# Optimization experiments

Hardware: AMD Instinct MI355X
Metric: run time of the kernel (lower is better)

Reference implementation:

```python
import jax, jax.numpy as jnp
import numpy as np

IN_F, OUT_F, R = 4096, 4096, 16
SCALING = 32.0 / R  # lora_alpha / r


def setup_inputs() -> dict:
    key = jax.random.key(0)
    kx, kw, kb, ka, kB = jax.random.split(key, 5)
    bound_w = 1.0 / np.sqrt(IN_F)  # kaiming_uniform a=sqrt(5) on (out,in) -> U(-1/sqrt(in), 1/sqrt(in))
    x = jax.random.normal(kx, (4, 4096, IN_F), dtype=jnp.float32)
    weight = jax.random.uniform(kw, (OUT_F, IN_F), jnp.float32, -bound_w, bound_w)
    bias = jax.random.uniform(kb, (OUT_F,), jnp.float32, -bound_w, bound_w)
    lora_A = jax.random.uniform(ka, (R, IN_F), jnp.float32, -bound_w, bound_w)
    # B is zero-init in the module; use small random values so the LoRA path is exercised
    lora_B = jax.random.normal(kB, (OUT_F, R), dtype=jnp.float32) * 0.01
    return {"x": x, "weight": weight, "bias": bias, "lora_A": lora_A, "lora_B": lora_B}


def reference(x, weight, bias, lora_A, lora_B):
    # base: F.linear(x, W, b) = x @ W.T + b
    base_out = jnp.einsum("bsi,oi->bso", x, weight) + bias
    # low-rank path: (x @ A.T) @ B.T * scaling  (dropout=0 -> identity)
    xr = jnp.einsum("bsi,ri->bsr", x, lora_A)  # [b, s, r]
    lora_out = jnp.einsum("bsr,or->bso", xr, lora_B) * SCALING
    return base_out + lora_out
```

## Files before the change

### kernel.cpp

```cpp
#include <hip/hip_runtime.h>
#include <hip/hip_bf16.h>


typedef __attribute__((ext_vector_type(8))) short bf16x8;
typedef __attribute__((ext_vector_type(4))) float f32x4;
typedef __attribute__((ext_vector_type(4))) unsigned short u16x4;

#define M_DIM 16384
#define N_DIM 4096
#define K_DIM 4096
#define NT 64

__device__ __forceinline__ unsigned short f2bf(float f) {
    unsigned int u = __builtin_bit_cast(unsigned int, f);
    unsigned int r = u + 0x7FFFu + ((u >> 16) & 1u);
    return (unsigned short)(r >> 16);
}

__device__ __forceinline__ void async16(const void* g, void* l) {
    __builtin_amdgcn_global_load_lds(
        (const __attribute__((address_space(1))) unsigned int*)g,
        (__attribute__((address_space(3))) unsigned int*)l,
        16, 0, 0);
}

__global__ void __launch_bounds__(256) cast_x_kernel(
    const float4* __restrict__ x, u16x4* __restrict__ y, int n4) {
    int i = blockIdx.x * blockDim.x + threadIdx.x;
    int stride = gridDim.x * blockDim.x;
    for (; i < n4; i += stride) {
        float4 v = x[i];
        u16x4 o = { f2bf(v.x), f2bf(v.y), f2bf(v.z), f2bf(v.w) };
        y[i] = o;
    }
}

__global__ void __launch_bounds__(256) weff_kernel(
    const float* __restrict__ W, const float* __restrict__ lA,
    const float* __restrict__ lB, unsigned short* __restrict__ out) {
    constexpr int K = K_DIM, R = 16;
    constexpr float S = 2.0f;
    int o = blockIdx.x;
    int t = threadIdx.x;
    float b[R];
#pragma unroll
    for (int r = 0; r < R; ++r) b[r] = lB[o * R + r];
#pragma unroll
    for (int c = 0; c < 4; ++c) {
        int i = c * 1024 + t * 4;
        float4 wv = *reinterpret_cast<const float4*>(&W[o * K + i]);
        float sx = 0.f, sy = 0.f, sz = 0.f, sw = 0.f;
#pragma unroll
        for (int r = 0; r < R; ++r) {
            float4 a = *reinterpret_cast<const float4*>(&lA[r * K + i]);
            sx += b[r] * a.x; sy += b[r] * a.y;
            sz += b[r] * a.z; sw += b[r] * a.w;
        }
        u16x4 ov = { f2bf(wv.x + S * sx), f2bf(wv.y + S * sy),
                     f2bf(wv.z + S * sz), f2bf(wv.w + S * sw) };
        *reinterpret_cast<u16x4*>(&out[o * K + i]) = ov;
    }
}

#define STAGE(G, h, tt, bsel, moff)                                           \
    do {                                                                      \
        const unsigned short* g0 = (G) +                                      \
            (size_t)((h) * 128 + wid * 16 + rc) * K_DIM + (tt) * 64 + cc * 8; \
        char* l0 = lds + (bsel) * 65536 + (moff) + (h) * 16384 + wid * 2048;  \
        async16(g0, l0);                                                      \
        async16(g0 + 8 * K_DIM, l0 + 1024);                                   \
    } while (0)

#define LDA_TO(dst, mh, bsel)                                                 \
    _Pragma("unroll") for (int mm = 0; mm < 4; ++mm)                          \
    _Pragma("unroll") for (int ks = 0; ks < 2; ++ks)                          \
        dst[mm][ks] = *(const bf16x8*)(lds + (bsel) * 65536 +                 \
            ((aBase + ((mh) * 4 + mm) * 2048) ^ (ks << 6)));

#define LDB_TO(nh, bsel)                                                      \
    _Pragma("unroll") for (int nn = 0; nn < 2; ++nn)                          \
    _Pragma("unroll") for (int ks = 0; ks < 2; ++ks)                          \
        br[(nh) * 2 + nn][ks] = *(const bf16x8*)(lds + (bsel) * 65536 +       \
            ((bBase + ((nh) * 2 + nn) * 2048) ^ (ks << 6)));

#define MM_Q(src, mh, nh)                                                     \
    __builtin_amdgcn_s_setprio(1);                                            \
    _Pragma("unroll") for (int ks = 0; ks < 2; ++ks)                          \
    _Pragma("unroll") for (int mm = 0; mm < 4; ++mm)                          \
    _Pragma("unroll") for (int nn = 0; nn < 2; ++nn)                          \
        acc[(mh) * 4 + mm][(nh) * 2 + nn] =                                   \
            __builtin_amdgcn_mfma_f32_16x16x32_bf16(                          \
                src[mm][ks], br[(nh) * 2 + nn][ks],                           \
                acc[(mh) * 4 + mm][(nh) * 2 + nn], 0, 0, 0);                  \
    __builtin_amdgcn_s_setprio(0)

#define CFENCE() asm volatile("" ::: "memory")

#define KTILE(t)                                                              \
    {                                                                         \
        const int bs_ = (t) & 1, bo_ = bs_ ^ 1;                               \
        if ((t) + 1 < NT) {                                                   \
            STAGE(Ag, 0, (t) + 1, bo_, 0);                                    \
            STAGE(Ag, 1, (t) + 1, bo_, 0);                                    \
        }                                                                     \
        LDA_TO(ar, 0, bs_);                                                   \
        LDB_TO(0, bs_);                                                       \
        LDB_TO(1, bs_);                                                       \
        MM_Q(ar, 0, 0);                                                       \
        MM_Q(ar, 0, 1);                                                       \
        CFENCE();                                                             \
        __builtin_amdgcn_s_barrier();                                         \
        CFENCE();                                                             \
        if ((t) + 2 < NT) STAGE(Bg, 0, (t) + 2, bs_, 32768);                  \
        LDA_TO(ar, 1, bs_);                                                   \
        MM_Q(ar, 1, 0);                                                       \
        if ((t) + 2 < NT) STAGE(Bg, 1, (t) + 2, bs_, 32768);                  \
        MM_Q(ar, 1, 1);                                                       \
        if ((t) < NT - 2) {                                                   \
            asm volatile("s_waitcnt vmcnt(4)" ::: "memory");                  \
        } else {                                                              \
            asm volatile("s_waitcnt vmcnt(0)" ::: "memory");                  \
        }                                                                     \
        __builtin_amdgcn_s_barrier();                                         \
        CFENCE();                                                             \
    }

__global__ void __launch_bounds__(512, 2) gemm2b_kernel(
    const unsigned short* __restrict__ A,
    const unsigned short* __restrict__ B,
    const float* __restrict__ bias,
    float* __restrict__ C) {
    __shared__ __align__(1024) char lds[131072];

    const int tid = threadIdx.x;
    const int lane = tid & 63, wid = tid >> 6;
    const int wm = wid >> 2, wn = wid & 3;
    const int lr = lane & 15, lg = lane >> 4;

    const int bid = blockIdx.x;
    const int swz = (bid & 7) * 128 + (bid >> 3);
    const int bm = swz >> 4, bn = swz & 15;

    const unsigned short* Ag = A + (size_t)bm * 256 * K_DIM;
    const unsigned short* Bg = B + (size_t)bn * 256 * K_DIM;

    const int lam = lane ^ (lane >> 3);
    const int rc = lam >> 3, cc = lam & 7;

    const int kx0 = (lg * 16) ^ ((lr & 7) << 4);
    const int aBase = (wm * 128 + lr) * 128 + kx0;
    const int bBase = 32768 + (wn * 64 + lr) * 128 + kx0;

    f32x4 acc[8][4] = {};
    bf16x8 ar[4][2], br[4][2];

    STAGE(Bg, 0, 0, 0, 32768);
    STAGE(Bg, 1, 0, 0, 32768);
    STAGE(Ag, 0, 0, 0, 0);
    STAGE(Ag, 1, 0, 0, 0);
    STAGE(Bg, 0, 1, 1, 32768);
    STAGE(Bg, 1, 1, 1, 32768);
    asm volatile("s_waitcnt vmcnt(4)" ::: "memory");
    __builtin_amdgcn_s_barrier();
    CFENCE();

#pragma unroll 2
    for (int t = 0; t < NT; ++t) {
        KTILE(t);
    }

    const int row0 = bm * 256 + wm * 128;
    const int col0 = bn * 256 + wn * 64;
#pragma unroll
    for (int n = 0; n < 4; ++n) {
        const int col = col0 + n * 16 + lr;
        const float bv = bias[col];
#pragma unroll
        for (int m = 0; m < 8; ++m) {
            const int r0 = row0 + m * 16 + lg * 4;
#pragma unroll
            for (int r = 0; r < 4; ++r)
                C[(size_t)(r0 + r) * N_DIM + col] = acc[m][n][r] + bv;
        }
    }
}

extern "C" void kernel_launch(void* const* d_in, const int* in_sizes, int n_in,
                              void* d_out, int out_size, void* d_ws, size_t ws_size,
                              hipStream_t stream) {
    const float* x    = (const float*)d_in[0];
    const float* W    = (const float*)d_in[1];
    const float* bias = (const float*)d_in[2];
    const float* lA   = (const float*)d_in[3];
    const float* lB   = (const float*)d_in[4];
    float* out = (float*)d_out;

    unsigned short* xb   = (unsigned short*)d_ws;
    unsigned short* weff = (unsigned short*)((char*)d_ws + 134217728);

    cast_x_kernel<<<2048, 256, 0, stream>>>((const float4*)x, (u16x4*)xb,
                                            M_DIM * K_DIM / 4);
    weff_kernel<<<N_DIM, 256, 0, stream>>>(W, lA, lB, weff);
    gemm2b_kernel<<<(M_DIM / 256) * (N_DIM / 256), 512, 0, stream>>>(
        xb, weff, bias, out);
}
```

Before: 593.6 us.

## Split GEMM inner loop by k-slice with fine-grained LDS waits to overlap reads and MFMA

Restructures the per-tile schedule so LDS fragment reads are issued per k-slice and interleaved with MFMA groups. Explicit lgkmcnt waits with sched_barrier let compute start once part of the data has arrived. A operands are kept in two alternating register sets so loads for the next group overlap the current group's math. The aim is to hide LDS latency behind matrix ops, at the cost of a more fragile hand schedule and possibly higher register pressure.

Measured after the change: 593.2 us (median of 2 runs). Within noise of the previous version (-0.1%).

```diff
diff --git a/kernel.cpp b/kernel.cpp
--- a/kernel.cpp
+++ b/kernel.cpp
@@ -71,51 +71,53 @@
         async16(g0 + 8 * K_DIM, l0 + 1024);                                   \
     } while (0)
 
-#define LDA_TO(dst, mh, bsel)                                                 \
+#define LDA_KS(dst, mh, ks, bsel)                                             \
     _Pragma("unroll") for (int mm = 0; mm < 4; ++mm)                          \
-    _Pragma("unroll") for (int ks = 0; ks < 2; ++ks)                          \
-        dst[mm][ks] = *(const bf16x8*)(lds + (bsel) * 65536 +                 \
-            ((aBase + ((mh) * 4 + mm) * 2048) ^ (ks << 6)));
-
-#define LDB_TO(nh, bsel)                                                      \
-    _Pragma("unroll") for (int nn = 0; nn < 2; ++nn)                          \
-    _Pragma("unroll") for (int ks = 0; ks < 2; ++ks)                          \
-        br[(nh) * 2 + nn][ks] = *(const bf16x8*)(lds + (bsel) * 65536 +       \
-            ((bBase + ((nh) * 2 + nn) * 2048) ^ (ks << 6)));
-
-#define MM_Q(src, mh, nh)                                                     \
+        dst[mm] = *(const bf16x8*)(lds + (bsel) * 65536 +                     \
+            ((aBase + ((mh) * 4 + mm) * 2048) ^ ((ks) << 6)));
+
+#define LDB_KS(ks, bsel)                                                      \
+    _Pragma("unroll") for (int nn = 0; nn < 4; ++nn)                          \
+        br[nn][ks] = *(const bf16x8*)(lds + (bsel) * 65536 +                  \
+            ((bBase + nn * 2048) ^ ((ks) << 6)));
+
+#define MMQ_KS(src, mh, ks)                                                   \
     __builtin_amdgcn_s_setprio(1);                                            \
-    _Pragma("unroll") for (int ks = 0; ks < 2; ++ks)                          \
     _Pragma("unroll") for (int mm = 0; mm < 4; ++mm)                          \
-    _Pragma("unroll") for (int nn = 0; nn < 2; ++nn)                          \
-        acc[(mh) * 4 + mm][(nh) * 2 + nn] =                                   \
-            __builtin_amdgcn_mfma_f32_16x16x32_bf16(                          \
-                src[mm][ks], br[(nh) * 2 + nn][ks],                           \
-                acc[(mh) * 4 + mm][(nh) * 2 + nn], 0, 0, 0);                  \
+    _Pragma("unroll") for (int nn = 0; nn < 4; ++nn)                          \
+        acc[(mh) * 4 + mm][nn] = __builtin_amdgcn_mfma_f32_16x16x32_bf16(     \
+            src[mm], br[nn][ks], acc[(mh) * 4 + mm][nn], 0, 0, 0);            \
     __builtin_amdgcn_s_setprio(0)
 
 #define CFENCE() asm volatile("" ::: "memory")
+#define WAIT_LGKM(n)                                                          \
+    asm volatile("s_waitcnt lgkmcnt(" #n ")" ::: "memory");                   \
+    __builtin_amdgcn_sched_barrier(0)
 
 #define KTILE(t)                                                              \
     {                                                                         \
         const int bs_ = (t) & 1, bo_ = bs_ ^ 1;                               \
-        if ((t) + 1 < NT) {                                                   \
-            STAGE(Ag, 0, (t) + 1, bo_, 0);                                    \
-            STAGE(Ag, 1, (t) + 1, bo_, 0);                                    \
-        }                                                                     \
-        LDA_TO(ar, 0, bs_);                                                   \
-        LDB_TO(0, bs_);                                                       \
-        LDB_TO(1, bs_);                                                       \
-        MM_Q(ar, 0, 0);                                                       \
-        MM_Q(ar, 0, 1);                                                       \
+        LDA_KS(arE, 0, 0, bs_);                                   \
+        LDB_KS(0, bs_);                                           \
+        if ((t) + 1 < NT) STAGE(Ag, 0, (t) + 1, bo_, 0);                      \
+        LDA_KS(arO, 1, 0, bs_);                                    \
+        WAIT_LGKM(4);                                                         \
+        MMQ_KS(arE, 0, 0);                                                    \
+        if ((t) + 1 < NT) STAGE(Ag, 1, (t) + 1, bo_, 0);                      \
+        LDA_KS(arE, 0, 1, bs_);                \
+        LDB_KS(1, bs_);                                           \
+        WAIT_LGKM(8);                                                         \
+        MMQ_KS(arO, 1, 0);                                                    \
+        LDA_KS(arO, 1, 1, bs_);                                    \
+        WAIT_LGKM(4);                                                         \
+        MMQ_KS(arE, 0, 1);                                                    \
         CFENCE();                                                             \
-        __builtin_amdgcn_s_barrier();                                         \
+        __builtin_amdgcn_s_barrier();    \
         CFENCE();                                                             \
         if ((t) + 2 < NT) STAGE(Bg, 0, (t) + 2, bs_, 32768);                  \
-        LDA_TO(ar, 1, bs_);                                                   \
-        MM_Q(ar, 1, 0);                                                       \
+        WAIT_LGKM(0);                                                         \
+        MMQ_KS(arO, 1, 1);                                                    \
         if ((t) + 2 < NT) STAGE(Bg, 1, (t) + 2, bs_, 32768);                  \
-        MM_Q(ar, 1, 1);                                                       \
         if ((t) < NT - 2) {                                                   \
             asm volatile("s_waitcnt vmcnt(4)" ::: "memory");                  \
         } else {                                                              \
@@ -125,7 +127,7 @@
         CFENCE();                                                             \
     }
 
-__global__ void __launch_bounds__(512, 2) gemm2b_kernel(
+__global__ void __launch_bounds__(512, 2) gemmks_kernel(
     const unsigned short* __restrict__ A,
     const unsigned short* __restrict__ B,
     const float* __restrict__ bias,
@@ -152,7 +154,7 @@
     const int bBase = 32768 + (wn * 64 + lr) * 128 + kx0;
 
     f32x4 acc[8][4] = {};
-    bf16x8 ar[4][2], br[4][2];
+    bf16x8 arE[4], arO[4], br[4][2];
 
     STAGE(Bg, 0, 0, 0, 32768);
     STAGE(Bg, 1, 0, 0, 32768);
@@ -201,6 +203,6 @@
     cast_x_kernel<<<2048, 256, 0, stream>>>((const float4*)x, (u16x4*)xb,
                                             M_DIM * K_DIM / 4);
     weff_kernel<<<N_DIM, 256, 0, stream>>>(W, lA, lB, weff);
-    gemm2b_kernel<<<(M_DIM / 256) * (N_DIM / 256), 512, 0, stream>>>(
+    gemmks_kernel<<<(M_DIM / 256) * (N_DIM / 256), 512, 0, stream>>>(
         xb, weff, bias, out);
 }
```
